# Kernel tuning notes

Measured on AMD Instinct MI355X. Metric: run time of the kernel, lower is better.

The kernel has to match this reference:

```python
import jax, jax.numpy as jnp
import numpy as np

KS = 3      # deform/standard conv kernel size
PAD = 1     # padding == dilation == 1
EPS = 1e-5  # BatchNorm eps


def conv2d(x, w, b, stride=1, padding=0):
    out = jax.lax.conv_general_dilated(
        x, w, (stride, stride), [(padding, padding), (padding, padding)],
        dimension_numbers=('NCHW', 'OIHW', 'NCHW'))
    return out + b[None, :, None, None]


def bn_relu(x, bn):
    gamma, beta, mean, var = bn[0], bn[1], bn[2], bn[3]
    inv = gamma / jnp.sqrt(var + EPS)
    y = x * inv[None, :, None, None] + (beta - mean * inv)[None, :, None, None]
    return jax.nn.relu(y)


def _gather(xp_flat, qx, qy, Wp, c):
    # xp_flat: (b, c, Hp*Wp); qx, qy: (b, h, w, N) int32 -> (b, c, h, w, N)
    b = qx.shape[0]
    idx = (qx * Wp + qy).reshape(b, 1, -1)
    out = jnp.take_along_axis(xp_flat, jnp.broadcast_to(idx, (b, c, idx.shape[-1])), axis=2)
    return out.reshape(b, c, *qx.shape[1:])


def deform_conv(x, w_off, b_off, w_def, b_def, stride=1):
    b, c, H, W = x.shape
    N = KS * KS
    offset = conv2d(x, w_off, b_off, stride=stride, padding=1)  # (b, 2N, h, w)
    h, w = offset.shape[2], offset.shape[3]
    xp = jnp.pad(x, ((0, 0), (0, 0), (PAD, PAD), (PAD, PAD)))
    Hp, Wp = H + 2 * PAD, W + 2 * PAD
    r = (KS - 1) // 2
    pn_x, pn_y = jnp.meshgrid(jnp.arange(-r, r + 1), jnp.arange(-r, r + 1), indexing='ij')
    p_n = jnp.concatenate([pn_x.ravel(), pn_y.ravel()]).astype(x.dtype)  # (2N,)
    p0_x = jnp.arange(1, h * stride + 1, stride, dtype=x.dtype)
    p0_y = jnp.arange(1, w * stride + 1, stride, dtype=x.dtype)
    p0 = jnp.concatenate([jnp.broadcast_to(p0_x[None, :, None], (N, h, w)),
                          jnp.broadcast_to(p0_y[None, None, :], (N, h, w))], 0)
    p = (offset + p_n[None, :, None, None] + p0[None]).transpose(0, 2, 3, 1)  # (b,h,w,2N)
    q = jnp.floor(jax.lax.stop_gradient(p))
    lt_x = jnp.clip(q[..., :N], 0, Hp - 1); lt_y = jnp.clip(q[..., N:], 0, Wp - 1)
    rb_x = jnp.clip(q[..., :N] + 1, 0, Hp - 1); rb_y = jnp.clip(q[..., N:] + 1, 0, Wp - 1)
    p_x = jnp.clip(p[..., :N], 0, Hp - 1); p_y = jnp.clip(p[..., N:], 0, Wp - 1)
    g_lt = (1 + (lt_x - p_x)) * (1 + (lt_y - p_y))
    g_rb = (1 - (rb_x - p_x)) * (1 - (rb_y - p_y))
    g_lb = (1 + (lt_x - p_x)) * (1 - (rb_y - p_y))
    g_rt = (1 - (rb_x - p_x)) * (1 + (lt_y - p_y))
    xpf = xp.reshape(b, c, -1)
    ii = lambda t: t.astype(jnp.int32)
    x_lt = _gather(xpf, ii(lt_x), ii(lt_y), Wp, c)
    x_rb = _gather(xpf, ii(rb_x), ii(rb_y), Wp, c)
    x_lb = _gather(xpf, ii(lt_x), ii(rb_y), Wp, c)
    x_rt = _gather(xpf, ii(rb_x), ii(lt_y), Wp, c)
    x_off = (g_lt[:, None] * x_lt + g_rb[:, None] * x_rb +
             g_lb[:, None] * x_lb + g_rt[:, None] * x_rt)  # (b, c, h, w, N)
    # (b,c,h,w,ks_i,ks_j) -> (b,c,h*ks,w*ks), N ordered row-major (i*ks+j)
    x_off = x_off.reshape(b, c, h, w, KS, KS).transpose(0, 1, 2, 4, 3, 5).reshape(b, c, h * KS, w * KS)
    return conv2d(x_off, w_def, b_def, stride=KS, padding=0)


def setup_inputs() -> dict:
    key = jax.random.key(0)
    ks = jax.random.split(key, 16)
    B, Cin, H, W = 4, 128, 96, 96
    C2, Cout = 128, 256
    s = 0.05
    bn = lambda k1, k2: jnp.stack([jnp.ones(C2, jnp.float32), jnp.zeros(C2, jnp.float32),
                                   jax.random.normal(k1, (C2,)) * 0.1,
                                   jax.random.uniform(k2, (C2,)) + 0.5])
    return {
        'x': jax.random.normal(ks[0], (B, Cin, H, W), jnp.float32),
        'w_in': jax.random.normal(ks[1], (C2, Cin, 1, 1)) * s,
        'b_in': jax.random.normal(ks[2], (C2,)) * s,
        'w_off': jax.random.normal(ks[3], (2 * KS * KS, C2, 3, 3)) * s,
        'b_off': jax.random.normal(ks[4], (2 * KS * KS,)) * s,
        'w_def': jax.random.normal(ks[5], (C2, C2, KS, KS)) * s,
        'b_def': jax.random.normal(ks[6], (C2,)) * s,
        'bn1': bn(ks[7], ks[8]),
        'w_std': jax.random.normal(ks[9], (C2, C2, 3, 3)) * s,
        'b_std': jax.random.normal(ks[10], (C2,)) * s,
        'bn2': bn(ks[11], ks[12]),
        'w_out': jax.random.normal(ks[13], (Cout, Cout, 1, 1)) * s,
        'b_out': jax.random.normal(ks[14], (Cout,)) * s,
    }


def reference(x, w_in, b_in, w_off, b_off, w_def, b_def, bn1, w_std, b_std, bn2, w_out, b_out):
    x_c = conv2d(x, w_in, b_in)                                    # 1x1 reduce to ch_out/2
    x1 = bn_relu(deform_conv(x_c, w_off, b_off, w_def, b_def), bn1)  # deformable branch
    x2 = bn_relu(conv2d(x_c, w_std, b_std, padding=1), bn2)       # standard 3x3 branch
    # stride == 1 path: concat(deform, std + residual) then 1x1 fuse
    return conv2d(jnp.concatenate([x1, x2 + x_c], axis=1), w_out, b_out)
```

## Files before the change

kernel.cpp:

```cpp
#include <hip/hip_runtime.h>
#include <hip/hip_bf16.h>

#define BB 4
#define CC 128
#define HH 96
#define WW 96
#define PX (HH*WW)
#define HP 98
#define WP 98
#define PP (HP*WP)
#define K2 1152
#define BN_EPS 1e-5f

typedef __hip_bfloat16 bf16;
typedef __attribute__((ext_vector_type(8))) short bf16x8;
typedef __attribute__((ext_vector_type(4))) float f32x4;
__device__ __forceinline__ float b2f(bf16 v) { return __bfloat162float(v); }
union F8 { bf16x8 v; bf16 h[8]; int4 i4; };

#define MFMA(a, b, c) __builtin_amdgcn_mfma_f32_16x16x32_bf16((a), (b), (c), 0, 0, 0)

__device__ __forceinline__ float ldin(const void* p, size_t i, int f) {
  return f ? ((const float*)p)[i] : b2f(((const bf16*)p)[i]);
}

#define P_BIN  0
#define P_BOFF 128
#define P_BDEF 160
#define P_BN1  288
#define P_BSTD 800
#define P_BN2  928
#define P_BOUT 1440

__global__ __launch_bounds__(256) void probe_params(
    const void* bn1, const void* b_in, const void* b_off, const void* b_def,
    const void* b_std, const void* bn2, const void* b_out,
    int* __restrict__ flag, float* __restrict__ prm) {
  int f = (((const unsigned*)bn1)[0] == 0x3F800000u) ? 1 : 0;
  if (threadIdx.x == 0) flag[0] = f;
  int t = threadIdx.x;
  if (t < 128) prm[P_BIN + t]  = ldin(b_in, t, f);
  if (t < 18)  prm[P_BOFF + t] = ldin(b_off, t, f);
  if (t < 128) prm[P_BDEF + t] = ldin(b_def, t, f);
  for (int i = t; i < 512; i += 256) prm[P_BN1 + i] = ldin(bn1, i, f);
  if (t < 128) prm[P_BSTD + t] = ldin(b_std, t, f);
  for (int i = t; i < 512; i += 256) prm[P_BN2 + i] = ldin(bn2, i, f);
  if (t < 256) prm[P_BOUT + t] = ldin(b_out, t, f);
}

__global__ __launch_bounds__(256) void prep_weights(
    const void* w_in, const void* w_def, const void* w_std, const void* w_out,
    const void* w_off,
    bf16* __restrict__ w_inB, bf16* __restrict__ w_defB,
    bf16* __restrict__ w_stdB, bf16* __restrict__ w_outB,
    bf16* __restrict__ w_offP, const int* __restrict__ flag) {
  int f = flag[0];
  int i = blockIdx.x * 256 + threadIdx.x;
  if (i < K2 * 128) {
    int o = i / K2, kk = i - o * K2;
    int c = kk / 9, n = kk - c * 9;
    int dst = o * K2 + n * 128 + c;
    w_defB[dst] = __float2bfloat16(ldin(w_def, i, f));
    w_stdB[dst] = __float2bfloat16(ldin(w_std, i, f));
  }
  if (i < 32 * K2) {
    int o = i / K2, kk = i - o * K2;
    int c = kk / 9, n = kk - c * 9;
    int dst = o * K2 + n * 128 + c;
    w_offP[dst] = (o < 18) ? __float2bfloat16(ldin(w_off, i, f))
                           : __float2bfloat16(0.f);
  }
  if (i < 128 * 128) w_inB[i]  = __float2bfloat16(ldin(w_in, i, f));
  if (i < 256 * 256) w_outB[i] = __float2bfloat16(ldin(w_out, i, f));
}

__global__ __launch_bounds__(256) void conv1x1_in(
    const void* __restrict__ x, const bf16* __restrict__ wB,
    const float* __restrict__ prm, bf16* __restrict__ xcT,
    const int* __restrict__ flag, int b0) {
  __shared__ bf16 ct[128][136];
  bf16 (*xt)[40] = (bf16(*)[40])ct;
  int f = flag[0];
  int tid = threadIdx.x;
  int p0 = blockIdx.x * 128;
  int bg = b0 + blockIdx.y, bl = blockIdx.y;
  int lane = tid & 63, wv = tid >> 6;
  int quad = lane >> 4, l16 = lane & 15;
  int krow = tid >> 3, pxs = (tid & 7) * 16;
  int sgrp = (tid & 7) & 3;
  f32x4 acc[2][8] = {};
  for (int k0 = 0; k0 < 128; k0 += 32) {
    union { bf16 h[16]; int4 i4[2]; } u;
    size_t base = (size_t)(bg * 128 + k0 + krow) * PX + p0 + pxs;
    if (f) {
      const float4* s = (const float4*)((const float*)x + base);
#pragma unroll
      for (int v = 0; v < 4; ++v) {
        float4 t = s[v];
        u.h[v * 4 + 0] = __float2bfloat16(t.x);
        u.h[v * 4 + 1] = __float2bfloat16(t.y);
        u.h[v * 4 + 2] = __float2bfloat16(t.z);
        u.h[v * 4 + 3] = __float2bfloat16(t.w);
      }
    } else {
      const int4* s = (const int4*)((const bf16*)x + base);
      u.i4[0] = s[0]; u.i4[1] = s[1];
    }
    int col = (((krow >> 3) ^ sgrp) << 3) | (krow & 7);
    __syncthreads();
#pragma unroll
    for (int j = 0; j < 16; ++j) xt[pxs + j][col] = u.h[j];
    __syncthreads();
    const bf16* wp = wB + (size_t)(wv * 32 + l16) * 128 + k0 + quad * 8;
    bf16x8 a0 = *(const bf16x8*)wp;
    bf16x8 a1 = *(const bf16x8*)(wp + 16 * 128);
#pragma unroll
    for (int p = 0; p < 8; ++p) {
      bf16x8 bfr = *(const bf16x8*)&xt[p * 16 + l16][(quad ^ (p & 3)) << 3];
      acc[0][p] = MFMA(a0, bfr, acc[0][p]);
      acc[1][p] = MFMA(a1, bfr, acc[1][p]);
    }
  }
  __syncthreads();
#pragma unroll
  for (int i = 0; i < 2; ++i)
#pragma unroll
    for (int r = 0; r < 4; ++r) {
      int o = wv * 32 + i * 16 + quad * 4 + r;
      float bs = prm[P_BIN + o];
#pragma unroll
      for (int p = 0; p < 8; ++p)
        ct[p * 16 + l16][o] = __float2bfloat16(acc[i][p][r] + bs);
    }
  __syncthreads();
  int px = tid >> 1, half = tid & 1;
  int gp = p0 + px;
  int h = gp / WW, w = gp - h * WW;
  bf16* dst = xcT + ((size_t)bl * PP + (size_t)(h + 1) * WP + (w + 1)) * CC + half * 64;
  const int4* src = (const int4*)&ct[px][half * 64];
#pragma unroll
  for (int j = 0; j < 8; ++j) ((int4*)dst)[j] = src[j];
}

__global__ __launch_bounds__(256) void conv_off_k(
    const bf16* __restrict__ xcT, const bf16* __restrict__ wP,
    const float* __restrict__ prm, float* __restrict__ off) {
  __shared__ bf16 xt[64][40];
  int tid = threadIdx.x;
  int p0 = blockIdx.x * 64;
  int bl = blockIdx.y;
  int lane = tid & 63, wv = tid >> 6;
  int quad = lane >> 4, l16 = lane & 15;
  int gpx = tid & 63, cq = tid >> 6;
  int gp = p0 + gpx;
  int gh = gp / WW, gw = gp - gh * WW;
  const bf16* xb = xcT + (size_t)bl * PP * CC;
  f32x4 acc0 = {}, acc1 = {};
  for (int ch = 0; ch < 36; ++ch) {
    int n = ch >> 2, c0 = (ch & 3) << 5;
    int ti = n / 3, tj = n - ti * 3;
    const bf16* wp = wP + (size_t)l16 * K2 + n * 128 + c0 + quad * 8;
    bf16x8 a0 = *(const bf16x8*)wp;
    bf16x8 a1 = *(const bf16x8*)(wp + 16 * K2);
    int4 v = *(const int4*)(xb + ((size_t)(gh + ti) * WP + gw + tj) * CC + c0 + cq * 8);
    __syncthreads();
    *(int4*)&xt[gpx][cq * 8] = v;
    __syncthreads();
    bf16x8 bfr = *(const bf16x8*)&xt[wv * 16 + l16][quad * 8];
    acc0 = MFMA(a0, bfr, acc0);
    acc1 = MFMA(a1, bfr, acc1);
  }
  int px = p0 + wv * 16 + l16;
#pragma unroll
  for (int r = 0; r < 4; ++r) {
    int o = quad * 4 + r;
    if (o < 18) off[((size_t)bl * 18 + o) * PX + px] = acc0[r] + prm[P_BOFF + o];
    int o1 = 16 + o;
    if (o1 < 18) off[((size_t)bl * 18 + o1) * PX + px] = acc1[r] + prm[P_BOFF + o1];
  }
}

__global__ __launch_bounds__(256) void deform_conv_k(
    const bf16* __restrict__ xcT, const float* __restrict__ off,
    const bf16* __restrict__ wB, const float* __restrict__ prm,
    bf16* __restrict__ ycat) {
  __shared__ int4   s_ofs[576];
  __shared__ float4 s_g[576];
  __shared__ bf16 xt[64][40];
  int tid = threadIdx.x;
  int p0 = blockIdx.x * 64;
  int bl = blockIdx.y;

  for (int it = tid; it < 576; it += 256) {
    int n = it >> 6, pl = it & 63;
    int p = p0 + pl;
    int h = p / WW, w = p - h * WW;
    float ox = off[(size_t)(bl * 18 + n) * PX + p];
    float oy = off[(size_t)(bl * 18 + 9 + n) * PX + p];
    float px = ox + (float)(n / 3 - 1) + (float)(h + 1);
    float py = oy + (float)(n % 3 - 1) + (float)(w + 1);
    float qx = floorf(px), qy = floorf(py);
    float ltx = fminf(fmaxf(qx, 0.f), (float)(HP - 1));
    float lty = fminf(fmaxf(qy, 0.f), (float)(WP - 1));
    float rbx = fminf(fmaxf(qx + 1.f, 0.f), (float)(HP - 1));
    float rby = fminf(fmaxf(qy + 1.f, 0.f), (float)(WP - 1));
    float pxc = fminf(fmaxf(px, 0.f), (float)(HP - 1));
    float pyc = fminf(fmaxf(py, 0.f), (float)(WP - 1));
    float ax = 1.f + (ltx - pxc), bx = 1.f - (rbx - pxc);
    float ay = 1.f + (lty - pyc), by = 1.f - (rby - pyc);
    int iltx = (int)ltx, ilty = (int)lty, irbx = (int)rbx, irby = (int)rby;
    s_ofs[it] = make_int4((iltx * WP + ilty) * (CC * 2), (irbx * WP + irby) * (CC * 2),
                          (iltx * WP + irby) * (CC * 2), (irbx * WP + ilty) * (CC * 2));
    s_g[it] = make_float4(ax * ay, bx * by, ax * by, bx * ay);
  }
  __syncthreads();

  int lane = tid & 63, wv = tid >> 6;
  int quad = lane >> 4, l16 = lane & 15;
  int gpx = tid & 63, cq = tid >> 6;
  const char* xbT = (const char*)(xcT + (size_t)bl * PP * CC);
  f32x4 acc[2][4] = {};
  int4 o4; float4 g4;
  for (int ch = 0; ch < 36; ++ch) {
    int n = ch >> 2, c0 = (ch & 3) << 5;
    const bf16* wp = wB + (size_t)(wv * 32 + l16) * K2 + n * 128 + c0 + quad * 8;
    bf16x8 a0 = *(const bf16x8*)wp;
    bf16x8 a1 = *(const bf16x8*)(wp + 16 * K2);
    if ((ch & 3) == 0) { o4 = s_ofs[n * 64 + gpx]; g4 = s_g[n * 64 + gpx]; }
    const char* cb = xbT + (size_t)(c0 + cq * 8) * 2;
    F8 A, B, C, D;
    A.v = *(const bf16x8*)(cb + o4.x);
    B.v = *(const bf16x8*)(cb + o4.y);
    C.v = *(const bf16x8*)(cb + o4.z);
    D.v = *(const bf16x8*)(cb + o4.w);
    F8 u;
#pragma unroll
    for (int j = 0; j < 8; ++j) {
      float v = g4.x * b2f(A.h[j]) + g4.y * b2f(B.h[j]) +
                g4.z * b2f(C.h[j]) + g4.w * b2f(D.h[j]);
      u.h[j] = __float2bfloat16(v);
    }
    __syncthreads();
    *(int4*)&xt[gpx][cq * 8] = u.i4;
    __syncthreads();
#pragma unroll
    for (int p = 0; p < 4; ++p) {
      bf16x8 bfr = *(const bf16x8*)&xt[p * 16 + l16][quad * 8];
      acc[0][p] = MFMA(a0, bfr, acc[0][p]);
      acc[1][p] = MFMA(a1, bfr, acc[1][p]);
    }
  }
#pragma unroll
  for (int i = 0; i < 2; ++i)
#pragma unroll
    for (int r = 0; r < 4; ++r) {
      int o = wv * 32 + i * 16 + quad * 4 + r;
      float bd = prm[P_BDEF + o];
      float g  = prm[P_BN1 + o],       be = prm[P_BN1 + 128 + o];
      float mn = prm[P_BN1 + 256 + o], vr = prm[P_BN1 + 384 + o];
      float inv = g / sqrtf(vr + BN_EPS);
      float add = be - mn * inv;
#pragma unroll
      for (int p = 0; p < 4; ++p) {
        int px = p0 + p * 16 + l16;
        float v = fmaxf((acc[i][p][r] + bd) * inv + add, 0.f);
        ycat[((size_t)bl * 256 + o) * PX + px] = __float2bfloat16(v);
      }
    }
}

__global__ __launch_bounds__(256) void std_conv_k(
    const bf16* __restrict__ xcT, const bf16* __restrict__ wB,
    const float* __restrict__ prm, bf16* __restrict__ ycat) {
  __shared__ bf16 xt[64][40];
  int tid = threadIdx.x;
  int p0 = blockIdx.x * 64;
  int bl = blockIdx.y;
  int lane = tid & 63, wv = tid >> 6;
  int quad = lane >> 4, l16 = lane & 15;
  int gpx = tid & 63, cq = tid >> 6;
  int gp = p0 + gpx;
  int gh = gp / WW, gw = gp - gh * WW;
  const bf16* xb = xcT + (size_t)bl * PP * CC;
  f32x4 acc[2][4] = {};
  for (int ch = 0; ch < 36; ++ch) {
    int n = ch >> 2, c0 = (ch & 3) << 5;
    int ti = n / 3, tj = n - ti * 3;
    const bf16* wp = wB + (size_t)(wv * 32 + l16) * K2 + n * 128 + c0 + quad * 8;
    bf16x8 a0 = *(const bf16x8*)wp;
    bf16x8 a1 = *(const bf16x8*)(wp + 16 * K2);
    int4 v = *(const int4*)(xb + ((size_t)(gh + ti) * WP + gw + tj) * CC + c0 + cq * 8);
    __syncthreads();
    *(int4*)&xt[gpx][cq * 8] = v;
    __syncthreads();
#pragma unroll
    for (int p = 0; p < 4; ++p) {
      bf16x8 bfr = *(const bf16x8*)&xt[p * 16 + l16][quad * 8];
      acc[0][p] = MFMA(a0, bfr, acc[0][p]);
      acc[1][p] = MFMA(a1, bfr, acc[1][p]);
    }
  }
#pragma unroll
  for (int i = 0; i < 2; ++i)
#pragma unroll
    for (int r = 0; r < 4; ++r) {
      int o = wv * 32 + i * 16 + quad * 4 + r;
      float bs = prm[P_BSTD + o];
      float g  = prm[P_BN2 + o],       be = prm[P_BN2 + 128 + o];
      float mn = prm[P_BN2 + 256 + o], vr = prm[P_BN2 + 384 + o];
      float inv = g / sqrtf(vr + BN_EPS);
      float add = be - mn * inv;
#pragma unroll
      for (int p = 0; p < 4; ++p) {
        int px = p0 + p * 16 + l16;
        int hh = px / WW, ww = px - hh * WW;
        float res = b2f(xb[((size_t)(hh + 1) * WP + ww + 1) * CC + o]);
        float v = fmaxf((acc[i][p][r] + bs) * inv + add, 0.f) + res;
        ycat[((size_t)bl * 256 + 128 + o) * PX + px] = __float2bfloat16(v);
      }
    }
}

__global__ __launch_bounds__(256) void conv1x1_out(
    const bf16* __restrict__ ycat, const bf16* __restrict__ wB,
    const float* __restrict__ prm, void* __restrict__ out,
    const int* __restrict__ flag, int b0) {
  __shared__ bf16 xt[128][40];
  int f = flag[0];
  int tid = threadIdx.x;
  int p0 = blockIdx.x * 128;
  int half = blockIdx.y;
  int bg = b0 + blockIdx.z, bl = blockIdx.z;
  int lane = tid & 63, wv = tid >> 6;
  int quad = lane >> 4, l16 = lane & 15;
  int krow = tid >> 3, pxs = (tid & 7) * 16;
  int sgrp = (tid & 7) & 3;
  const bf16* yb = ycat + (size_t)bl * 256 * PX;
  f32x4 acc[2][8] = {};
  for (int k0 = 0; k0 < 256; k0 += 32) {
    union { bf16 h[16]; int4 i4[2]; } u;
    const int4* s = (const int4*)(yb + (size_t)(k0 + krow) * PX + p0 + pxs);
    u.i4[0] = s[0]; u.i4[1] = s[1];
    int col = (((krow >> 3) ^ sgrp) << 3) | (krow & 7);
    __syncthreads();
#pragma unroll
    for (int j = 0; j < 16; ++j) xt[pxs + j][col] = u.h[j];
    __syncthreads();
    const bf16* wp = wB + (size_t)(half * 128 + wv * 32 + l16) * 256 + k0 + quad * 8;
    bf16x8 a0 = *(const bf16x8*)wp;
    bf16x8 a1 = *(const bf16x8*)(wp + 16 * 256);
#pragma unroll
    for (int p = 0; p < 8; ++p) {
      bf16x8 bfr = *(const bf16x8*)&xt[p * 16 + l16][(quad ^ (p & 3)) << 3];
      acc[0][p] = MFMA(a0, bfr, acc[0][p]);
      acc[1][p] = MFMA(a1, bfr, acc[1][p]);
    }
  }
#pragma unroll
  for (int i = 0; i < 2; ++i)
#pragma unroll
    for (int r = 0; r < 4; ++r) {
      int o = half * 128 + wv * 32 + i * 16 + quad * 4 + r;
      float bs = prm[P_BOUT + o];
#pragma unroll
      for (int p = 0; p < 8; ++p) {
        int px = p0 + p * 16 + l16;
        size_t idx = ((size_t)bg * 256 + o) * PX + px;
        float v = acc[i][p][r] + bs;
        if (f) ((float*)out)[idx] = v;
        else   ((bf16*)out)[idx] = __float2bfloat16(v);
      }
    }
}

extern "C" void kernel_launch(void* const* d_in, const int* in_sizes, int n_in,
                              void* d_out, int out_size, void* d_ws, size_t ws_size,
                              hipStream_t stream) {
  const void* x     = d_in[0];
  const void* w_in  = d_in[1];
  const void* b_in  = d_in[2];
  const void* w_off = d_in[3];
  const void* b_off = d_in[4];
  const void* w_def = d_in[5];
  const void* b_def = d_in[6];
  const void* bn1   = d_in[7];
  const void* w_std = d_in[8];
  const void* b_std = d_in[9];
  const void* bn2   = d_in[10];
  const void* w_out = d_in[11];
  const void* b_out = d_in[12];

  char* wsb = (char*)d_ws;
  int*   flag   = (int*)wsb;
  float* prm    = (float*)(wsb + 1024);
  bf16*  w_offP = (bf16*)(wsb + 8192);
  bf16*  w_inB  = (bf16*)(wsb + 91136);
  bf16*  w_defB = (bf16*)(wsb + 123904);
  bf16*  w_stdB = (bf16*)(wsb + 418816);
  bf16*  w_outB = (bf16*)(wsb + 713728);
  const size_t FIXED = 847872;

  const size_t XCB  = (size_t)CC * PP * sizeof(bf16);
  const size_t OFFB = (size_t)18 * PX * sizeof(float);
  const size_t YCB  = (size_t)256 * PX * sizeof(bf16);
  const size_t PERB = XCB + OFFB + YCB;
  int nb = 1;
  if (ws_size > FIXED) {
    size_t fit = (ws_size - FIXED) / PERB;
    nb = (int)(fit < 1 ? 1 : (fit > BB ? BB : fit));
  }
  bf16*  xcA  = (bf16*)(wsb + FIXED);
  float* offA = (float*)(wsb + FIXED + (size_t)nb * XCB);
  bf16*  ycA  = (bf16*)(wsb + FIXED + (size_t)nb * (XCB + OFFB));

  probe_params<<<1, 256, 0, stream>>>(bn1, b_in, b_off, b_def, b_std, bn2, b_out,
                                      flag, prm);
  hipMemsetAsync(xcA, 0, (size_t)nb * XCB, stream);

  prep_weights<<<(K2 * 128 + 255) / 256, 256, 0, stream>>>(
      w_in, w_def, w_std, w_out, w_off, w_inB, w_defB, w_stdB, w_outB, w_offP, flag);

  for (int b0 = 0; b0 < BB; b0 += nb) {
    int nz = (BB - b0) < nb ? (BB - b0) : nb;
    conv1x1_in<<<dim3(PX / 128, nz), 256, 0, stream>>>(
        x, w_inB, prm, xcA, flag, b0);
    conv_off_k<<<dim3(PX / 64, nz), 256, 0, stream>>>(
        xcA, w_offP, prm, offA);
    deform_conv_k<<<dim3(PX / 64, nz), 256, 0, stream>>>(
        xcA, offA, w_defB, prm, ycA);
    std_conv_k<<<dim3(PX / 64, nz), 256, 0, stream>>>(
        xcA, w_stdB, prm, ycA);
    conv1x1_out<<<dim3(PX / 128, 2, nz), 256, 0, stream>>>(
        ycA, w_outB, prm, d_out, flag, b0);
  }
}
```

Measured before the change: 290.6 us.

## Double-buffer LDS and prefetch next chunk in conv kernels with 32-pixel tiles

Restructures the offset, deformable and standard 3x3 conv kernels to use 128-thread blocks over 32-pixel tiles. Each wave now covers 64 output channels, and LDS staging is double-buffered so only one barrier per K-chunk is needed. The next chunk's activations, bilinear samples and weights are loaded into registers while the current chunk's MFMAs run, hiding global-load latency. The trade-offs are higher register pressure from holding a_c/a_n and the four gathered vectors, plus more blocks with less activation reuse per weight load.

```diff
diff --git a/kernel.cpp b/kernel.cpp
--- a/kernel.cpp
+++ b/kernel.cpp
@@ -142,57 +142,65 @@
   for (int j = 0; j < 8; ++j) ((int4*)dst)[j] = src[j];
 }
 
-__global__ __launch_bounds__(256) void conv_off_k(
+__global__ __launch_bounds__(128) void conv_off_k(
     const bf16* __restrict__ xcT, const bf16* __restrict__ wP,
     const float* __restrict__ prm, float* __restrict__ off) {
-  __shared__ bf16 xt[64][40];
+  __shared__ bf16 xt[2][32][40];
   int tid = threadIdx.x;
-  int p0 = blockIdx.x * 64;
+  int p0 = blockIdx.x * 32;
   int bl = blockIdx.y;
   int lane = tid & 63, wv = tid >> 6;
   int quad = lane >> 4, l16 = lane & 15;
-  int gpx = tid & 63, cq = tid >> 6;
+  int gpx = tid & 31, cq = tid >> 5;
   int gp = p0 + gpx;
   int gh = gp / WW, gw = gp - gh * WW;
   const bf16* xb = xcT + (size_t)bl * PP * CC;
-  f32x4 acc0 = {}, acc1 = {};
+  f32x4 acc[2] = {};
+  int4 vc, vn;
+  bf16x8 ac, an;
+  vc = *(const int4*)(xb + ((size_t)gh * WP + gw) * CC + cq * 8);
+  ac = *(const bf16x8*)(wP + (size_t)(wv * 16 + l16) * K2 + quad * 8);
   for (int ch = 0; ch < 36; ++ch) {
-    int n = ch >> 2, c0 = (ch & 3) << 5;
-    int ti = n / 3, tj = n - ti * 3;
-    const bf16* wp = wP + (size_t)l16 * K2 + n * 128 + c0 + quad * 8;
-    bf16x8 a0 = *(const bf16x8*)wp;
-    bf16x8 a1 = *(const bf16x8*)(wp + 16 * K2);
-    int4 v = *(const int4*)(xb + ((size_t)(gh + ti) * WP + gw + tj) * CC + c0 + cq * 8);
-    __syncthreads();
-    *(int4*)&xt[gpx][cq * 8] = v;
-    __syncthreads();
-    bf16x8 bfr = *(const bf16x8*)&xt[wv * 16 + l16][quad * 8];
-    acc0 = MFMA(a0, bfr, acc0);
-    acc1 = MFMA(a1, bfr, acc1);
-  }
-  int px = p0 + wv * 16 + l16;
-#pragma unroll
-  for (int r = 0; r < 4; ++r) {
-    int o = quad * 4 + r;
-    if (o < 18) off[((size_t)bl * 18 + o) * PX + px] = acc0[r] + prm[P_BOFF + o];
-    int o1 = 16 + o;
-    if (o1 < 18) off[((size_t)bl * 18 + o1) * PX + px] = acc1[r] + prm[P_BOFF + o1];
-  }
-}
-
-__global__ __launch_bounds__(256) void deform_conv_k(
+    if (ch + 1 < 36) {
+      int ch1 = ch + 1;
+      int n = ch1 >> 2, c0 = (ch1 & 3) << 5;
+      int ti = n / 3, tj = n - ti * 3;
+      vn = *(const int4*)(xb + ((size_t)(gh + ti) * WP + gw + tj) * CC + c0 + cq * 8);
+      an = *(const bf16x8*)(wP + (size_t)(wv * 16 + l16) * K2 + n * 128 + c0 + quad * 8);
+    }
+    *(int4*)&xt[ch & 1][gpx][cq * 8] = vc;
+    __syncthreads();
+#pragma unroll
+    for (int p = 0; p < 2; ++p) {
+      bf16x8 bfr = *(const bf16x8*)&xt[ch & 1][p * 16 + l16][quad * 8];
+      acc[p] = MFMA(ac, bfr, acc[p]);
+    }
+    vc = vn; ac = an;
+  }
+#pragma unroll
+  for (int p = 0; p < 2; ++p) {
+    int px = p0 + p * 16 + l16;
+#pragma unroll
+    for (int r = 0; r < 4; ++r) {
+      int o = wv * 16 + quad * 4 + r;
+      if (o < 18) off[((size_t)bl * 18 + o) * PX + px] = acc[p][r] + prm[P_BOFF + o];
+    }
+  }
+}
+
+__global__ __launch_bounds__(128) void deform_conv_k(
     const bf16* __restrict__ xcT, const float* __restrict__ off,
     const bf16* __restrict__ wB, const float* __restrict__ prm,
     bf16* __restrict__ ycat) {
-  __shared__ int4   s_ofs[576];
-  __shared__ float4 s_g[576];
-  __shared__ bf16 xt[64][40];
+  __shared__ int4   s_ofs[288];
+  __shared__ float4 s_g[288];
+  __shared__ bf16 xt[2][32][40];
   int tid = threadIdx.x;
-  int p0 = blockIdx.x * 64;
+  int p0 = blockIdx.x * 32;
   int bl = blockIdx.y;
 
-  for (int it = tid; it < 576; it += 256) {
-    int n = it >> 6, pl = it & 63;
+  for (int it = tid; it < 288; it += 128) {
+    int n = it >> 5, pl = it & 31;
     int p = p0 + pl;
     int h = p / WW, w = p - h * WW;
     float ox = off[(size_t)(bl * 18 + n) * PX + p];
@@ -217,105 +225,135 @@
 
   int lane = tid & 63, wv = tid >> 6;
   int quad = lane >> 4, l16 = lane & 15;
-  int gpx = tid & 63, cq = tid >> 6;
+  int gpx = tid & 31, cq = tid >> 5;
   const char* xbT = (const char*)(xcT + (size_t)bl * PP * CC);
-  f32x4 acc[2][4] = {};
-  int4 o4; float4 g4;
+  const bf16* wrow = wB + (size_t)(wv * 64 + l16) * K2 + quad * 8;
+  f32x4 acc[4][2] = {};
+  F8 Ac, Bc, Cc, Dc, An, Bn, Cn, Dn;
+  float4 g4c, g4n;
+  bf16x8 a_c[4], a_n[4];
+  {
+    int4 o4 = s_ofs[gpx];
+    g4c = s_g[gpx];
+    const char* cb = xbT + (size_t)(cq * 8) * 2;
+    Ac.v = *(const bf16x8*)(cb + o4.x);
+    Bc.v = *(const bf16x8*)(cb + o4.y);
+    Cc.v = *(const bf16x8*)(cb + o4.z);
+    Dc.v = *(const bf16x8*)(cb + o4.w);
+#pragma unroll
+    for (int s = 0; s < 4; ++s) a_c[s] = *(const bf16x8*)(wrow + (size_t)s * 16 * K2);
+  }
   for (int ch = 0; ch < 36; ++ch) {
-    int n = ch >> 2, c0 = (ch & 3) << 5;
-    const bf16* wp = wB + (size_t)(wv * 32 + l16) * K2 + n * 128 + c0 + quad * 8;
-    bf16x8 a0 = *(const bf16x8*)wp;
-    bf16x8 a1 = *(const bf16x8*)(wp + 16 * K2);
-    if ((ch & 3) == 0) { o4 = s_ofs[n * 64 + gpx]; g4 = s_g[n * 64 + gpx]; }
-    const char* cb = xbT + (size_t)(c0 + cq * 8) * 2;
-    F8 A, B, C, D;
-    A.v = *(const bf16x8*)(cb + o4.x);
-    B.v = *(const bf16x8*)(cb + o4.y);
-    C.v = *(const bf16x8*)(cb + o4.z);
-    D.v = *(const bf16x8*)(cb + o4.w);
+    if (ch + 1 < 36) {
+      int ch1 = ch + 1;
+      int n = ch1 >> 2, c0 = (ch1 & 3) << 5;
+      int4 o4 = s_ofs[n * 32 + gpx];
+      g4n = s_g[n * 32 + gpx];
+      const char* cb = xbT + (size_t)(c0 + cq * 8) * 2;
+      An.v = *(const bf16x8*)(cb + o4.x);
+      Bn.v = *(const bf16x8*)(cb + o4.y);
+      Cn.v = *(const bf16x8*)(cb + o4.z);
+      Dn.v = *(const bf16x8*)(cb + o4.w);
+#pragma unroll
+      for (int s = 0; s < 4; ++s)
+        a_n[s] = *(const bf16x8*)(wrow + n * 128 + c0 + (size_t)s * 16 * K2);
+    }
     F8 u;
 #pragma unroll
     for (int j = 0; j < 8; ++j) {
-      float v = g4.x * b2f(A.h[j]) + g4.y * b2f(B.h[j]) +
-                g4.z * b2f(C.h[j]) + g4.w * b2f(D.h[j]);
+      float v = g4c.x * b2f(Ac.h[j]) + g4c.y * b2f(Bc.h[j]) +
+                g4c.z * b2f(Cc.h[j]) + g4c.w * b2f(Dc.h[j]);
       u.h[j] = __float2bfloat16(v);
     }
-    __syncthreads();
-    *(int4*)&xt[gpx][cq * 8] = u.i4;
-    __syncthreads();
-#pragma unroll
-    for (int p = 0; p < 4; ++p) {
-      bf16x8 bfr = *(const bf16x8*)&xt[p * 16 + l16][quad * 8];
-      acc[0][p] = MFMA(a0, bfr, acc[0][p]);
-      acc[1][p] = MFMA(a1, bfr, acc[1][p]);
-    }
-  }
-#pragma unroll
-  for (int i = 0; i < 2; ++i)
+    *(int4*)&xt[ch & 1][gpx][cq * 8] = u.i4;
+    __syncthreads();
+#pragma unroll
+    for (int p = 0; p < 2; ++p) {
+      bf16x8 bfr = *(const bf16x8*)&xt[ch & 1][p * 16 + l16][quad * 8];
+#pragma unroll
+      for (int s = 0; s < 4; ++s) acc[s][p] = MFMA(a_c[s], bfr, acc[s][p]);
+    }
+    Ac = An; Bc = Bn; Cc = Cn; Dc = Dn; g4c = g4n;
+#pragma unroll
+    for (int s = 0; s < 4; ++s) a_c[s] = a_n[s];
+  }
+#pragma unroll
+  for (int s = 0; s < 4; ++s)
 #pragma unroll
     for (int r = 0; r < 4; ++r) {
-      int o = wv * 32 + i * 16 + quad * 4 + r;
+      int o = wv * 64 + s * 16 + quad * 4 + r;
       float bd = prm[P_BDEF + o];
       float g  = prm[P_BN1 + o],       be = prm[P_BN1 + 128 + o];
       float mn = prm[P_BN1 + 256 + o], vr = prm[P_BN1 + 384 + o];
       float inv = g / sqrtf(vr + BN_EPS);
       float add = be - mn * inv;
 #pragma unroll
-      for (int p = 0; p < 4; ++p) {
+      for (int p = 0; p < 2; ++p) {
         int px = p0 + p * 16 + l16;
-        float v = fmaxf((acc[i][p][r] + bd) * inv + add, 0.f);
+        float v = fmaxf((acc[s][p][r] + bd) * inv + add, 0.f);
         ycat[((size_t)bl * 256 + o) * PX + px] = __float2bfloat16(v);
       }
     }
 }
 
-__global__ __launch_bounds__(256) void std_conv_k(
+__global__ __launch_bounds__(128) void std_conv_k(
     const bf16* __restrict__ xcT, const bf16* __restrict__ wB,
     const float* __restrict__ prm, bf16* __restrict__ ycat) {
-  __shared__ bf16 xt[64][40];
+  __shared__ bf16 xt[2][32][40];
   int tid = threadIdx.x;
-  int p0 = blockIdx.x * 64;
+  int p0 = blockIdx.x * 32;
   int bl = blockIdx.y;
   int lane = tid & 63, wv = tid >> 6;
   int quad = lane >> 4, l16 = lane & 15;
-  int gpx = tid & 63, cq = tid >> 6;
+  int gpx = tid & 31, cq = tid >> 5;
   int gp = p0 + gpx;
   int gh = gp / WW, gw = gp - gh * WW;
   const bf16* xb = xcT + (size_t)bl * PP * CC;
-  f32x4 acc[2][4] = {};
+  const bf16* wrow = wB + (size_t)(wv * 64 + l16) * K2 + quad * 8;
+  f32x4 acc[4][2] = {};
+  int4 vc, vn;
+  bf16x8 a_c[4], a_n[4];
+  vc = *(const int4*)(xb + ((size_t)gh * WP + gw) * CC + cq * 8);
+#pragma unroll
+  for (int s = 0; s < 4; ++s) a_c[s] = *(const bf16x8*)(wrow + (size_t)s * 16 * K2);
   for (int ch = 0; ch < 36; ++ch) {
-    int n = ch >> 2, c0 = (ch & 3) << 5;
-    int ti = n / 3, tj = n - ti * 3;
-    const bf16* wp = wB + (size_t)(wv * 32 + l16) * K2 + n * 128 + c0 + quad * 8;
-    bf16x8 a0 = *(const bf16x8*)wp;
-    bf16x8 a1 = *(const bf16x8*)(wp + 16 * K2);
-    int4 v = *(const int4*)(xb + ((size_t)(gh + ti) * WP + gw + tj) * CC + c0 + cq * 8);
-    __syncthreads();
-    *(int4*)&xt[gpx][cq * 8] = v;
-    __syncthreads();
-#pragma unroll
-    for (int p = 0; p < 4; ++p) {
-      bf16x8 bfr = *(const bf16x8*)&xt[p * 16 + l16][quad * 8];
-      acc[0][p] = MFMA(a0, bfr, acc[0][p]);
-      acc[1][p] = MFMA(a1, bfr, acc[1][p]);
-    }
-  }
-#pragma unroll
-  for (int i = 0; i < 2; ++i)
+    if (ch + 1 < 36) {
+      int ch1 = ch + 1;
+      int n = ch1 >> 2, c0 = (ch1 & 3) << 5;
+      int ti = n / 3, tj = n - ti * 3;
+      vn = *(const int4*)(xb + ((size_t)(gh + ti) * WP + gw + tj) * CC + c0 + cq * 8);
+#pragma unroll
+      for (int s = 0; s < 4; ++s)
+        a_n[s] = *(const bf16x8*)(wrow + n * 128 + c0 + (size_t)s * 16 * K2);
+    }
+    *(int4*)&xt[ch & 1][gpx][cq * 8] = vc;
+    __syncthreads();
+#pragma unroll
+    for (int p = 0; p < 2; ++p) {
+      bf16x8 bfr = *(const bf16x8*)&xt[ch & 1][p * 16 + l16][quad * 8];
+#pragma unroll
+      for (int s = 0; s < 4; ++s) acc[s][p] = MFMA(a_c[s], bfr, acc[s][p]);
+    }
+    vc = vn;
+#pragma unroll
+    for (int s = 0; s < 4; ++s) a_c[s] = a_n[s];
+  }
+#pragma unroll
+  for (int s = 0; s < 4; ++s)
 #pragma unroll
     for (int r = 0; r < 4; ++r) {
-      int o = wv * 32 + i * 16 + quad * 4 + r;
+      int o = wv * 64 + s * 16 + quad * 4 + r;
       float bs = prm[P_BSTD + o];
       float g  = prm[P_BN2 + o],       be = prm[P_BN2 + 128 + o];
       float mn = prm[P_BN2 + 256 + o], vr = prm[P_BN2 + 384 + o];
       float inv = g / sqrtf(vr + BN_EPS);
       float add = be - mn * inv;
 #pragma unroll
-      for (int p = 0; p < 4; ++p) {
+      for (int p = 0; p < 2; ++p) {
         int px = p0 + p * 16 + l16;
         int hh = px / WW, ww = px - hh * WW;
         float res = b2f(xb[((size_t)(hh + 1) * WP + ww + 1) * CC + o]);
-        float v = fmaxf((acc[i][p][r] + bs) * inv + add, 0.f) + res;
+        float v = fmaxf((acc[s][p][r] + bs) * inv + add, 0.f) + res;
         ycat[((size_t)bl * 256 + 128 + o) * PX + px] = __float2bfloat16(v);
       }
     }
@@ -424,11 +462,11 @@
     int nz = (BB - b0) < nb ? (BB - b0) : nb;
     conv1x1_in<<<dim3(PX / 128, nz), 256, 0, stream>>>(
         x, w_inB, prm, xcA, flag, b0);
-    conv_off_k<<<dim3(PX / 64, nz), 256, 0, stream>>>(
+    conv_off_k<<<dim3(PX / 32, nz), 128, 0, stream>>>(
         xcA, w_offP, prm, offA);
-    deform_conv_k<<<dim3(PX / 64, nz), 256, 0, stream>>>(
+    deform_conv_k<<<dim3(PX / 32, nz), 128, 0, stream>>>(
         xcA, offA, w_defB, prm, ycA);
-    std_conv_k<<<dim3(PX / 64, nz), 256, 0, stream>>>(
+    std_conv_k<<<dim3(PX / 32, nz), 128, 0, stream>>>(
         xcA, w_stdB, prm, ycA);
     conv1x1_out<<<dim3(PX / 128, 2, nz), 256, 0, stream>>>(
         ycA, w_outB, prm, d_out, flag, b0);
```

Result: no change. 293.9 us (+1.1%).
